# Performance work log

Measured on AMD Instinct MI355X. Metric: run time of the kernel, lower is better.

Reference implementation:

```python
import jax, jax.numpy as jnp
import numpy as np
from jax import lax

B, C, H, W = 8, 4, 256, 256
INF = jnp.float32(1e6)  # > any possible distance on the grid; INF**2 safe in fp32


def _dist1d_to_zero(mask):
    """1D distance along the last axis to the nearest background (False) pixel.

    mask: [N, H, W] bool, True = foreground. Returns float32 [N, H, W].
    """
    def step(carry, z):  # carry, z: [N, H]
        d = jnp.where(z, carry + 1.0, 0.0)
        return d, d

    zT = jnp.moveaxis(mask, -1, 0)                      # [W, N, H]
    init = jnp.full(mask.shape[:-1], INF, jnp.float32)  # [N, H]
    _, left = lax.scan(step, init, zT)                  # scan left -> right
    _, right = lax.scan(step, init, zT, reverse=True)   # scan right -> left
    g = jnp.minimum(left, right)                        # [W, N, H]
    return jnp.moveaxis(g, 0, -1)                       # [N, H, W]


def _edt2d(mask):
    """Exact 2D Euclidean distance transform (Felzenszwalb-Huttenlocher style,
    vectorized envelope). mask: [N, H, W] bool. Returns float32 [N, H, W]."""
    g = _dist1d_to_zero(mask)   # per-row 1D distance to nearest zero
    g2 = g * g                  # [N, H, W]
    i = jnp.arange(mask.shape[-2], dtype=jnp.float32)
    dk2 = (i[:, None] - i[None, :]) ** 2  # [H, H] squared row offsets

    def combine(g2_img):  # g2_img: [H, W] -> exact squared EDT [H, W]
        # D2[i, j] = min_k ( (i - k)^2 + g(k, j)^2 )
        return jnp.min(dk2[:, :, None] + g2_img[None, :, :], axis=1)

    # lax.map keeps the [H, H, W] intermediate to one image at a time (~64 MB)
    d2 = lax.map(combine, g2)
    return jnp.sqrt(d2)


def setup_inputs() -> dict:
    key = jax.random.key(0)
    x = jax.random.randint(key, (B, C, H, W), 0, 2).astype(jnp.float32)
    return {"x": x}


def reference(x):
    # scipy edt treats any nonzero (incl. NaN) as foreground
    mask = (x != 0) | jnp.isnan(x)                    # [B, C, H, W]
    flat = mask.reshape(B * C, H, W)
    dist = _edt2d(flat).reshape(B, C, H, W)
    # positions that were NaN in the input are set back to NaN
    return jnp.where(jnp.isnan(x), jnp.nan, dist)
```

## Files before the change

kernel.cpp:

```cpp
#include <hip/hip_runtime.h>
#include <math.h>

#define NIMG 32
#define H 256
#define W 256
#define RWIN 16
#define PANEL_ROWS (64 + 2*RWIN)

__global__ __launch_bounds__(256) void edt_rows(const float* __restrict__ x,
                                                float* __restrict__ g2) {
    const int lane = threadIdx.x & 63;
    const int wv   = threadIdx.x >> 6;
    const int row  = blockIdx.x * 4 + wv;

    const float4 v = reinterpret_cast<const float4*>(x + (size_t)row * W)[lane];
    const int base = lane * 4;

    bool bgs[4];
    bgs[0] = (v.x == 0.0f);
    bgs[1] = (v.y == 0.0f);
    bgs[2] = (v.z == 0.0f);
    bgs[3] = (v.w == 0.0f);

    int lanelast = -1;
    #pragma unroll
    for (int e = 0; e < 4; ++e) if (bgs[e]) lanelast = base + e;

    int s = lanelast;
    #pragma unroll
    for (int off = 1; off < 64; off <<= 1) {
        int t = __shfl_up(s, off);
        if (lane >= off) s = max(s, t);
    }
    int excl_last = __shfl_up(s, 1);
    if (lane == 0) excl_last = -1;

    const int BIG = 1 << 29;
    int lanefirst = BIG;
    #pragma unroll
    for (int e = 3; e >= 0; --e) if (bgs[e]) lanefirst = base + e;

    int s2 = lanefirst;
    #pragma unroll
    for (int off = 1; off < 64; off <<= 1) {
        int t = __shfl_down(s2, off);
        if (lane + off < 64) s2 = min(s2, t);
    }
    int excl_first = __shfl_down(s2, 1);
    if (lane == 63) excl_first = BIG;

    float dl[4], dr[4];
    int cur = excl_last;
    #pragma unroll
    for (int e = 0; e < 4; ++e) {
        int w = base + e;
        if (bgs[e]) { dl[e] = 0.0f; cur = w; }
        else        { dl[e] = (cur < 0) ? 1.0e6f : (float)(w - cur); }
    }
    int cur2 = excl_first;
    #pragma unroll
    for (int e = 3; e >= 0; --e) {
        int w = base + e;
        if (bgs[e]) { dr[e] = 0.0f; cur2 = w; }
        else        { dr[e] = (cur2 >= BIG) ? 1.0e6f : (float)(cur2 - w); }
    }

    float4 o;
    float a;
    a = fminf(dl[0], dr[0]); o.x = a * a;
    a = fminf(dl[1], dr[1]); o.y = a * a;
    a = fminf(dl[2], dr[2]); o.z = a * a;
    a = fminf(dl[3], dr[3]); o.w = a * a;
    reinterpret_cast<float4*>(g2 + (size_t)row * W)[lane] = o;
}

__global__ __launch_bounds__(256) void edt_cols(const float* __restrict__ g2,
                                                const float* __restrict__ x,
                                                float* __restrict__ out) {
    __shared__ float sg2[PANEL_ROWS * 64];

    const int b    = blockIdx.x;
    const int img  = b >> 4;
    const int rem  = b & 15;
    const int i0   = (rem >> 2) * 64;
    const int c0   = (rem & 3) * 64;

    const float* gbase = g2 + (size_t)img * (H * W) + c0;

    for (int idx = threadIdx.x; idx < PANEL_ROWS * 64; idx += 256) {
        int srow = idx >> 6;
        int c    = idx & 63;
        int k    = i0 - RWIN + srow;
        float vk = (k >= 0 && k < H) ? gbase[(size_t)k * W + c] : 1.0e12f;
        sg2[idx] = vk;
    }
    __syncthreads();

    const int c     = threadIdx.x & 63;
    const int ig    = threadIdx.x >> 6;
    const int ibase = i0 + ig * 16;

    float best[16];
    #pragma unroll
    for (int m = 0; m < 16; ++m) best[m] = 3.0e38f;

    const int srow0 = ig * 16;
    #pragma unroll 4
    for (int t = 0; t < 2 * RWIN + 16; ++t) {
        float ld = sg2[(srow0 + t) * 64 + c];
        float dt = (float)(RWIN - t);
        #pragma unroll
        for (int m = 0; m < 16; ++m) {
            float diff = dt + (float)m;
            best[m] = fminf(best[m], fmaf(diff, diff, ld));
        }
    }

    const float thr = (float)((RWIN + 1) * (RWIN + 1));
    bool needExt = false;
    #pragma unroll
    for (int m = 0; m < 16; ++m) needExt |= (best[m] > thr);

    if (__syncthreads_count(needExt ? 1 : 0) != 0) {
        #pragma unroll 4
        for (int k = 0; k < H; ++k) {
            float ld = gbase[(size_t)k * W + c];
            float dk = (float)(ibase - k);
            #pragma unroll
            for (int m = 0; m < 16; ++m) {
                float diff = dk + (float)m;
                best[m] = fminf(best[m], fmaf(diff, diff, ld));
            }
        }
    }

    const int ocol = c0 + c;
    #pragma unroll
    for (int m = 0; m < 16; ++m) {
        int i   = ibase + m;
        size_t idx = (size_t)img * (H * W) + (size_t)i * W + ocol;
        float xv = x[idx];
        out[idx] = (xv != xv) ? xv : sqrtf(best[m]);
    }
}

extern "C" void kernel_launch(void* const* d_in, const int* in_sizes, int n_in,
                              void* d_out, int out_size, void* d_ws, size_t ws_size,
                              hipStream_t stream) {
    const float* x  = (const float*)d_in[0];
    float* out      = (float*)d_out;
    float* g2       = (float*)d_ws;

    edt_rows<<<dim3((NIMG * H) / 4), dim3(256), 0, stream>>>(x, g2);

    edt_cols<<<dim3(NIMG * 16), dim3(256), 0, stream>>>(g2, x, out);
}
```

Measured before the change: 78.21 us.

## Fuse row scan into column pass, recomputing row distances per panel

Merges the two kernels into one. Each block recomputes the row-wise 1D distances for the 96 rows it needs directly from the input and writes only its 64-column slice into shared memory, so the g2 workspace round trip and the second launch go away. The cost is redundant work: each block scans full 256-wide rows to keep 64 columns, about four times the row-scan compute. The rare fallback over all rows now restages chunks through shared memory instead of reading g2 from global memory.

```diff
diff --git a/kernel.cpp b/kernel.cpp
--- a/kernel.cpp
+++ b/kernel.cpp
@@ -5,15 +5,11 @@
 #define H 256
 #define W 256
 #define RWIN 16
-#define PANEL_ROWS (64 + 2*RWIN)
+#define PROWS 96
 
-__global__ __launch_bounds__(256) void edt_rows(const float* __restrict__ x,
-                                                float* __restrict__ g2) {
-    const int lane = threadIdx.x & 63;
-    const int wv   = threadIdx.x >> 6;
-    const int row  = blockIdx.x * 4 + wv;
-
-    const float4 v = reinterpret_cast<const float4*>(x + (size_t)row * W)[lane];
+__device__ __forceinline__ float4 row_scan_g2(const float* __restrict__ xrow,
+                                              int lane) {
+    const float4 v = reinterpret_cast<const float4*>(xrow)[lane];
     const int base = lane * 4;
 
     bool bgs[4];
@@ -25,7 +21,6 @@
     int lanelast = -1;
     #pragma unroll
     for (int e = 0; e < 4; ++e) if (bgs[e]) lanelast = base + e;
-
     int s = lanelast;
     #pragma unroll
     for (int off = 1; off < 64; off <<= 1) {
@@ -39,7 +34,6 @@
     int lanefirst = BIG;
     #pragma unroll
     for (int e = 3; e >= 0; --e) if (bgs[e]) lanefirst = base + e;
-
     int s2 = lanefirst;
     #pragma unroll
     for (int off = 1; off < 64; off <<= 1) {
@@ -65,39 +59,54 @@
         else        { dr[e] = (cur2 >= BIG) ? 1.0e6f : (float)(cur2 - w); }
     }
 
-    float4 o;
-    float a;
+    float4 o; float a;
     a = fminf(dl[0], dr[0]); o.x = a * a;
     a = fminf(dl[1], dr[1]); o.y = a * a;
     a = fminf(dl[2], dr[2]); o.z = a * a;
     a = fminf(dl[3], dr[3]); o.w = a * a;
-    reinterpret_cast<float4*>(g2 + (size_t)row * W)[lane] = o;
+    return o;
 }
 
-__global__ __launch_bounds__(256) void edt_cols(const float* __restrict__ g2,
-                                                const float* __restrict__ x,
-                                                float* __restrict__ out) {
-    __shared__ float sg2[PANEL_ROWS * 64];
+__device__ __forceinline__ void stage_chunk(float* __restrict__ sg2,
+                                            const float* __restrict__ ximg,
+                                            int kb, int c0, int lane, int wv) {
+    const int wcol    = lane * 4 - c0;
+    const bool writer = (wcol >= 0) && (wcol < 64);
+    #pragma unroll
+    for (int j = 0; j < PROWS / 8; ++j) {
+        const int r0 = wv + 4 * (2 * j);
+        const int r1 = wv + 4 * (2 * j + 1);
+        const int k0 = kb + r0, k1 = kb + r1;
+        float4 g0 = make_float4(1.0e12f, 1.0e12f, 1.0e12f, 1.0e12f);
+        float4 g1 = g0;
+        if (k0 >= 0 && k0 < H) g0 = row_scan_g2(ximg + (size_t)k0 * W, lane);
+        if (k1 >= 0 && k1 < H) g1 = row_scan_g2(ximg + (size_t)k1 * W, lane);
+        if (writer) {
+            *reinterpret_cast<float4*>(&sg2[r0 * 64 + wcol]) = g0;
+            *reinterpret_cast<float4*>(&sg2[r1 * 64 + wcol]) = g1;
+        }
+    }
+}
+
+__global__ __launch_bounds__(256) void edt_fused(const float* __restrict__ x,
+                                                 float* __restrict__ out) {
+    __shared__ float sg2[PROWS * 64];
 
     const int b    = blockIdx.x;
     const int img  = b >> 4;
     const int rem  = b & 15;
     const int i0   = (rem >> 2) * 64;
     const int c0   = (rem & 3) * 64;
+    const int lane = threadIdx.x & 63;
+    const int wv   = threadIdx.x >> 6;
 
-    const float* gbase = g2 + (size_t)img * (H * W) + c0;
+    const float* ximg = x + (size_t)img * (H * W);
 
-    for (int idx = threadIdx.x; idx < PANEL_ROWS * 64; idx += 256) {
-        int srow = idx >> 6;
-        int c    = idx & 63;
-        int k    = i0 - RWIN + srow;
-        float vk = (k >= 0 && k < H) ? gbase[(size_t)k * W + c] : 1.0e12f;
-        sg2[idx] = vk;
-    }
+    stage_chunk(sg2, ximg, i0 - RWIN, c0, lane, wv);
     __syncthreads();
 
-    const int c     = threadIdx.x & 63;
-    const int ig    = threadIdx.x >> 6;
+    const int c     = lane;
+    const int ig    = wv;
     const int ibase = i0 + ig * 16;
 
     float best[16];
@@ -122,14 +131,19 @@
     for (int m = 0; m < 16; ++m) needExt |= (best[m] > thr);
 
     if (__syncthreads_count(needExt ? 1 : 0) != 0) {
-        #pragma unroll 4
-        for (int k = 0; k < H; ++k) {
-            float ld = gbase[(size_t)k * W + c];
-            float dk = (float)(ibase - k);
-            #pragma unroll
-            for (int m = 0; m < 16; ++m) {
-                float diff = dk + (float)m;
-                best[m] = fminf(best[m], fmaf(diff, diff, ld));
+        for (int kb = 0; kb < H; kb += PROWS) {
+            __syncthreads();
+            stage_chunk(sg2, ximg, kb, c0, lane, wv);
+            __syncthreads();
+            #pragma unroll 4
+            for (int t = 0; t < PROWS; ++t) {
+                float ld = sg2[t * 64 + c];
+                float dk = (float)(ibase - (kb + t));
+                #pragma unroll
+                for (int m = 0; m < 16; ++m) {
+                    float diff = dk + (float)m;
+                    best[m] = fminf(best[m], fmaf(diff, diff, ld));
+                }
             }
         }
     }
@@ -137,21 +151,19 @@
     const int ocol = c0 + c;
     #pragma unroll
     for (int m = 0; m < 16; ++m) {
-        int i   = ibase + m;
+        int i      = ibase + m;
         size_t idx = (size_t)img * (H * W) + (size_t)i * W + ocol;
-        float xv = x[idx];
-        out[idx] = (xv != xv) ? xv : sqrtf(best[m]);
+        float xv   = x[idx];
+        out[idx]   = (xv != xv) ? xv : sqrtf(best[m]);
     }
 }
 
 extern "C" void kernel_launch(void* const* d_in, const int* in_sizes, int n_in,
                               void* d_out, int out_size, void* d_ws, size_t ws_size,
                               hipStream_t stream) {
-    const float* x  = (const float*)d_in[0];
-    float* out      = (float*)d_out;
-    float* g2       = (float*)d_ws;
+    const float* x = (const float*)d_in[0];
+    float* out     = (float*)d_out;
+    (void)d_ws; (void)ws_size;
 
-    edt_rows<<<dim3((NIMG * H) / 4), dim3(256), 0, stream>>>(x, g2);
-
-    edt_cols<<<dim3(NIMG * 16), dim3(256), 0, stream>>>(g2, x, out);
+    edt_fused<<<dim3(NIMG * 16), dim3(256), 0, stream>>>(x, out);
 }
```

New measurement: 82.14 us. 1.05x slower.
